# Performance work log

Measured on AMD Instinct MI355X. Metric: run time of the kernel, lower is better.

The kernel has to match this reference:

```python
import jax, jax.numpy as jnp
import numpy as np

N_NODES = 4
EPS = 1e-12


def gcn_conv(x, edge_index, W, b):
    B, N, _ = x.shape
    loop = jnp.arange(N)
    src = jnp.concatenate([edge_index[0], loop])
    dst = jnp.concatenate([edge_index[1], loop])
    deg = jnp.zeros((N,), x.dtype).at[dst].add(1.0)  # in-degree incl. self loops (>=1)
    dinv = jax.lax.rsqrt(deg)
    norm = dinv[src] * dinv[dst]                      # [E+N]
    h = jnp.einsum('bnf,fo->bno', x, W)               # transform first (out < ... ok)
    msgs = h[:, src, :] * norm[None, :, None]         # gather + edge weight
    out = jnp.zeros((B, N, W.shape[1]), x.dtype).at[:, dst, :].add(msgs)  # scatter-add
    return out + b


def sage_conv(x, edge_index, Wl, bl, Wr):
    # PyG SAGEConv(aggr='mean', normalize=True): out = lin_l(mean_j x_j) + lin_r(x_i), l2-normalized
    B, N, F = x.shape
    src, dst = edge_index[0], edge_index[1]
    cnt = jnp.zeros((N,), x.dtype).at[dst].add(1.0)
    cnt = jnp.maximum(cnt, 1.0)
    agg = jnp.zeros((B, N, F), x.dtype).at[:, dst, :].add(x[:, src, :])
    agg = agg / cnt[None, :, None]                    # mean neighbor aggregation
    out = jnp.einsum('bnf,fo->bno', agg, Wl) + bl + jnp.einsum('bnf,fo->bno', x, Wr)
    nrm = jnp.sqrt(jnp.sum(out * out, axis=-1, keepdims=True))
    return out / jnp.maximum(nrm, EPS)


def setup_inputs() -> dict:
    key = jax.random.key(0)
    ks = jax.random.split(key, 16)
    B, N, Cin, Cout = 32768, N_NODES, 64, 10
    E = 12

    def glorot(k, fi, fo):
        s = (6.0 / (fi + fo)) ** 0.5
        return jax.random.uniform(k, (fi, fo), jnp.float32, -s, s)

    x = jax.random.normal(ks[0], (B, N, Cin), jnp.float32)
    edge_index = jax.random.randint(ks[1], (2, E), 0, N, jnp.int64)
    inp = {
        'x': x, 'edge_index': edge_index,
        'W1': glorot(ks[2], Cin, 1024), 'b1': jnp.zeros((1024,), jnp.float32),
        'Wl2': glorot(ks[3], 1024, 512), 'bl2': jnp.zeros((512,), jnp.float32), 'Wr2': glorot(ks[4], 1024, 512),
        'Wl3': glorot(ks[5], 512, 256), 'bl3': jnp.zeros((256,), jnp.float32), 'Wr3': glorot(ks[6], 512, 256),
        'Wl4': glorot(ks[7], 256, 256), 'bl4': jnp.zeros((256,), jnp.float32), 'Wr4': glorot(ks[8], 256, 256),
        'Wfc': glorot(ks[9], N * 256, Cout), 'bfc': jnp.zeros((Cout,), jnp.float32),
    }
    return inp


def reference(x, edge_index, W1, b1, Wl2, bl2, Wr2, Wl3, bl3, Wr3, Wl4, bl4, Wr4, Wfc, bfc):
    h = jax.nn.relu(gcn_conv(x, edge_index, W1, b1))
    h = jax.nn.relu(sage_conv(h, edge_index, Wl2, bl2, Wr2))
    h = jax.nn.relu(sage_conv(h, edge_index, Wl3, bl3, Wr3))
    h = jax.nn.relu(sage_conv(h, edge_index, Wl4, bl4, Wr4))
    h = h.reshape(h.shape[0], -1)                     # [B, 4*256]
    logits = h @ Wfc + bfc
    return jax.nn.softmax(logits, axis=-1)
```

## Files before the change

kernel.cpp:

```cpp
#include <hip/hip_runtime.h>
#include <stdint.h>
#include <math.h>

typedef __bf16 bf16;
typedef __attribute__((ext_vector_type(8))) __bf16 bf16x8;
typedef __attribute__((ext_vector_type(16))) float f32x16;

#define AS1 __attribute__((address_space(1)))
#define AS3 __attribute__((address_space(3)))

__device__ __forceinline__ void glds16(const void* g, void* l) {
    __builtin_amdgcn_global_load_lds((const AS1 uint32_t*)g, (AS3 uint32_t*)l, 16, 0, 0);
}


__global__ void k_setup(const int* __restrict__ ei, float* __restrict__ gmat) {
    if (threadIdx.x != 0 || blockIdx.x != 0) return;
    bool is64 = true;
    for (int i = 0; i < 12; i++) if (ei[2 * i + 1] != 0) { is64 = false; break; }
    int src[12], dst[12];
    for (int e = 0; e < 12; e++) {
        if (is64) { src[e] = ei[2 * e]; dst[e] = ei[24 + 2 * e]; }
        else      { src[e] = ei[e];     dst[e] = ei[12 + e]; }
    }
    float deg[4] = {1.f, 1.f, 1.f, 1.f};
    for (int e = 0; e < 12; e++) deg[dst[e]] += 1.f;
    float dinv[4];
    for (int n = 0; n < 4; n++) dinv[n] = 1.f / sqrtf(deg[n]);
    float A[16];
    for (int i = 0; i < 16; i++) A[i] = 0.f;
    for (int e = 0; e < 12; e++) A[dst[e] * 4 + src[e]] += dinv[src[e]] * dinv[dst[e]];
    for (int n = 0; n < 4; n++) A[n * 4 + n] += dinv[n] * dinv[n];
    float cnt[4] = {0.f, 0.f, 0.f, 0.f};
    for (int e = 0; e < 12; e++) cnt[dst[e]] += 1.f;
    for (int n = 0; n < 4; n++) cnt[n] = fmaxf(cnt[n], 1.f);
    float Mm[16];
    for (int i = 0; i < 16; i++) Mm[i] = 0.f;
    for (int e = 0; e < 12; e++) Mm[dst[e] * 4 + src[e]] += 1.f;
    for (int n = 0; n < 4; n++)
        for (int m = 0; m < 4; m++) Mm[n * 4 + m] /= cnt[n];
    for (int i = 0; i < 16; i++) { gmat[i] = A[i]; gmat[16 + i] = Mm[i]; }
}

__global__ __launch_bounds__(256) void wtransF(const float* __restrict__ W, int K,
                                               int N, bf16* __restrict__ Wt) {
    int a = blockIdx.x * 256 + threadIdx.x;
    if (a >= N * K) return;
    int j = a & 7, c64 = (a >> 3) & 63, tile = a >> 9;
    int m32 = c64 & 31, kh = c64 >> 5;
    int TK = K >> 4;
    int rblk = tile / TK, ks = tile - rblk * TK;
    int n = rblk * 32 + m32, k = ks * 16 + kh * 8 + j;
    Wt[a] = (bf16)W[(size_t)k * N + n];
}

__global__ __launch_bounds__(256) void wtransI(const float* __restrict__ Wl,
                                               const float* __restrict__ Wr,
                                               int K, int F, bf16* __restrict__ Bt) {
    int a = blockIdx.x * 256 + threadIdx.x;
    if (a >= 2 * F * K) return;
    int j = a & 7, c64 = (a >> 3) & 63, tile = a >> 9;
    int m32 = c64 & 31, kh = c64 >> 5;
    int TK = K >> 4;
    int rblk = tile / TK, ks = tile - rblk * TK;
    int n = rblk * 32 + m32, k = ks * 16 + kh * 8 + j;
    int f = n >> 1;
    float v = (n & 1) ? Wr[(size_t)k * F + f] : Wl[(size_t)k * F + f];
    Bt[a] = (bf16)v;
}

__global__ __launch_bounds__(256) void cast_x(const float4* __restrict__ x,
                                              bf16x8* __restrict__ out) {
    int i = blockIdx.x * 256 + threadIdx.x;
    int c64 = i & 63, m32 = c64 & 31, kh = c64 >> 5;
    int tile = i >> 6, RB = tile >> 2, ks = tile & 3;
    int row = RB * 32 + m32;
    int fb4 = ks * 4 + kh * 2;
    float4 a = x[(size_t)row * 16 + fb4], b = x[(size_t)row * 16 + fb4 + 1];
    bf16x8 o;
    o[0] = (bf16)a.x; o[1] = (bf16)a.y; o[2] = (bf16)a.z; o[3] = (bf16)a.w;
    o[4] = (bf16)b.x; o[5] = (bf16)b.y; o[6] = (bf16)b.z; o[7] = (bf16)b.w;
    out[i] = o;
}

__global__ __launch_bounds__(256) void k_zero(float4* __restrict__ p, int n4) {
    int i = blockIdx.x * 256 + threadIdx.x;
    if (i < n4) p[i] = make_float4(0.f, 0.f, 0.f, 0.f);
}

__global__ __launch_bounds__(512, 2) void gemm_mfma(
    const bf16* __restrict__ A, int K,
    const bf16* __restrict__ Bt,
    const float* __restrict__ bias,
    bf16* __restrict__ out, int N, int mode,
    const float* __restrict__ gm, float* __restrict__ ssq) {
    __shared__ bf16 sA[2][16384];
    __shared__ bf16 sB[2][16384];
    const int t = threadIdx.x;
    const int lane = t & 63;
    const int w = t >> 6;
    const int wr = w >> 2, wc = w & 3;
    const int lin = blockIdx.x + gridDim.x * blockIdx.y;
    const int C = gridDim.x;
    const int xcd = lin & 7;
    const int seq = lin >> 3;
    const int rloc = seq / C;
    const int cloc = seq - rloc * C;
    const int row0 = (xcd + 8 * rloc) * 256;
    const int col0 = cloc * 256;
    const int m32 = lane & 31;
    const int kh = lane >> 5;

    f32x16 acc[4][2] = {};

    const int TK = K >> 4;
    const int le = lane * 8;
    const bf16* gA = A  + (size_t)((row0 >> 5) + w) * TK * 512 + le;
    const bf16* gB = Bt + (size_t)((col0 >> 5) + w) * TK * 512 + le;

    const int NT = K >> 6;
#pragma unroll
    for (int p = 0; p < 4; p++) {
        glds16(gA + p * 512, &sA[0][(p * 8 + w) * 512]);
        glds16(gB + p * 512, &sB[0][(p * 8 + w) * 512]);
    }

    for (int kt = 0; kt < NT; kt++) {
        const int rb = kt & 1;
        const size_t knext = (size_t)(kt + 1 < NT ? kt + 1 : kt) * 2048;
        asm volatile("s_waitcnt vmcnt(0)" ::: "memory");
        __builtin_amdgcn_s_barrier();
        asm volatile("" ::: "memory");
        bf16* dA = &sA[rb ^ 1][w * 512];
        bf16* dB = &sB[rb ^ 1][w * 512];
#pragma unroll
        for (int p = 0; p < 4; p++) {
            glds16(gA + knext + p * 512, dA + p * 8 * 512);
            glds16(gB + knext + p * 512, dB + p * 8 * 512);
        }
        const bf16* rA = &sA[rb][0];
        const bf16* rB = &sB[rb][0];
        __builtin_amdgcn_s_setprio(1);
#pragma unroll
        for (int p = 0; p < 4; p++) {
            bf16x8 af[4], bfr[2];
#pragma unroll
            for (int i = 0; i < 4; i++)
                af[i] = *(const bf16x8*)&rA[(p * 8 + wr * 4 + i) * 512 + le];
#pragma unroll
            for (int j = 0; j < 2; j++)
                bfr[j] = *(const bf16x8*)&rB[(p * 8 + wc * 2 + j) * 512 + le];
#pragma unroll
            for (int i = 0; i < 4; i++)
#pragma unroll
                for (int j = 0; j < 2; j++)
                    acc[i][j] = __builtin_amdgcn_mfma_f32_32x32x16_bf16(af[i], bfr[j], acc[i][j], 0, 0, 0);
        }
        __builtin_amdgcn_s_setprio(0);
    }
    asm volatile("s_waitcnt vmcnt(0)" ::: "memory");

    float g[16];
#pragma unroll
    for (int q = 0; q < 16; q++) g[q] = gm[q];

    if (mode == 1) {
        const int Tn = N >> 4;
#pragma unroll
        for (int i = 0; i < 4; i++) {
            size_t RBo = (size_t)(row0 >> 5) + 4 * wr + i;
#pragma unroll
            for (int j = 0; j < 2; j++) {
                int c = col0 + (2 * wc + j) * 32 + m32;
                size_t tbase = (RBo * Tn + (c >> 4)) * 512;
                int coff = ((c >> 3) & 1) * 32;
                int cj = c & 7;
                float bsv = bias[c];
#pragma unroll
                for (int q = 0; q < 4; q++) {
#pragma unroll
                    for (int n = 0; n < 4; n++) {
                        float v = g[n * 4 + 0] * acc[i][j][q * 4 + 0] +
                                  g[n * 4 + 1] * acc[i][j][q * 4 + 1] +
                                  g[n * 4 + 2] * acc[i][j][q * 4 + 2] +
                                  g[n * 4 + 3] * acc[i][j][q * 4 + 3] + bsv;
                        out[tbase + (size_t)(coff + 4 * kh + 8 * q + n) * 8 + cj] =
                            (bf16)fmaxf(v, 0.f);
                    }
                }
            }
        }
    } else {
        const int F = N >> 1;
        const int Tf = F >> 4;
        const bool ev = ((m32 & 1) == 0);
#pragma unroll
        for (int i = 0; i < 4; i++) {
            size_t RBo = (size_t)(row0 >> 5) + 4 * wr + i;
            int rbAbs = row0 + (4 * wr + i) * 32 + 4 * kh;
#pragma unroll
            for (int q = 0; q < 4; q++) {
                float ssql[4] = {0.f, 0.f, 0.f, 0.f};
#pragma unroll
                for (int j = 0; j < 2; j++) {
                    int c = col0 + (2 * wc + j) * 32 + m32;
                    int f = c >> 1;
                    size_t tbase = (RBo * Tf + (f >> 4)) * 512;
                    int foff = ((f >> 3) & 1) * 32;
                    int fj = f & 7;
                    float bsv = bias[f];
                    float mine[4];
                    if (ev) {
#pragma unroll
                        for (int n = 0; n < 4; n++)
                            mine[n] = g[n * 4 + 0] * acc[i][j][q * 4 + 0] +
                                      g[n * 4 + 1] * acc[i][j][q * 4 + 1] +
                                      g[n * 4 + 2] * acc[i][j][q * 4 + 2] +
                                      g[n * 4 + 3] * acc[i][j][q * 4 + 3];
                    } else {
#pragma unroll
                        for (int n = 0; n < 4; n++) mine[n] = acc[i][j][q * 4 + n];
                    }
#pragma unroll
                    for (int n = 0; n < 4; n++) {
                        float oth = __shfl_xor(mine[n], 1);
                        float tot = mine[n] + oth + bsv;
                        ssql[n] += tot * tot;
                        if (ev)
                            out[tbase + (size_t)(foff + 4 * kh + 8 * q + n) * 8 + fj] =
                                (bf16)tot;
                    }
                }
#pragma unroll
                for (int n = 0; n < 4; n++) {
                    float v = ssql[n];
                    v += __shfl_xor(v, 1); v += __shfl_xor(v, 2);
                    v += __shfl_xor(v, 4); v += __shfl_xor(v, 8);
                    v += __shfl_xor(v, 16);
                    ssql[n] = v;
                }
                if (m32 == 0) {
#pragma unroll
                    for (int n = 0; n < 4; n++)
                        atomicAdd(&ssq[rbAbs + 8 * q + n], ssql[n] * 0.5f);
                }
            }
        }
    }
}

__global__ __launch_bounds__(256) void norm_apply(bf16x8* __restrict__ h,
                                                  const float* __restrict__ ssq,
                                                  int tsh) {
    int idx = blockIdx.x * 256 + threadIdx.x;
    int row = (((idx >> 6) >> tsh) << 5) | (idx & 31);
    float inv = 1.f / fmaxf(sqrtf(ssq[row]), 1e-12f);
    bf16x8 v = h[idx], o;
#pragma unroll
    for (int c = 0; c < 8; c++) o[c] = (bf16)fmaxf((float)v[c] * inv, 0.f);
    h[idx] = o;
}

__global__ __launch_bounds__(256) void fc_softmax(const bf16x8* __restrict__ h,
                                                  const float* __restrict__ ssq4,
                                                  const float* __restrict__ Wfc,
                                                  const float* __restrict__ bfc,
                                                  float* __restrict__ outp) {
    __shared__ float WT[10][1024];
    int t = threadIdx.x;
    for (int i = t; i < 10240; i += 256) { int o = i % 10, k = i / 10; WT[o][k] = Wfc[i]; }
    __syncthreads();
    int wid = t >> 6, lane = t & 63;
    size_t e = (size_t)blockIdx.x * 4 + wid;
    size_t eb8 = e >> 3;
    int eo = (int)(e & 7);
    int ks = lane & 15, node = lane >> 4;
    float inv = 1.f / fmaxf(sqrtf(ssq4[e * 4 + node]), 1e-12f);
    float acc[10];
#pragma unroll
    for (int o = 0; o < 10; o++) acc[o] = 0.f;
#pragma unroll
    for (int jj = 0; jj < 2; jj++) {
        size_t ch = (eb8 * 16 + ks) * 64 + jj * 32 + eo * 4 + node;
        bf16x8 v = h[ch];
        float f[8];
#pragma unroll
        for (int c = 0; c < 8; c++) f[c] = fmaxf((float)v[c] * inv, 0.f);
        int k0 = node * 256 + ks * 16 + jj * 8;
#pragma unroll
        for (int o = 0; o < 10; o++) {
            const float* wr = &WT[o][k0];
            float s = 0.f;
#pragma unroll
            for (int c = 0; c < 8; c++) s += f[c] * wr[c];
            acc[o] += s;
        }
    }
#pragma unroll
    for (int o = 0; o < 10; o++) {
        float v = acc[o];
        v += __shfl_xor(v, 32); v += __shfl_xor(v, 16); v += __shfl_xor(v, 8);
        v += __shfl_xor(v, 4);  v += __shfl_xor(v, 2);  v += __shfl_xor(v, 1);
        acc[o] = v + bfc[o];
    }
    float mx = acc[0];
#pragma unroll
    for (int o = 1; o < 10; o++) mx = fmaxf(mx, acc[o]);
    float sum = 0.f, p[10];
#pragma unroll
    for (int o = 0; o < 10; o++) { p[o] = expf(acc[o] - mx); sum += p[o]; }
    float inv2 = 1.f / sum;
    if (lane < 10) outp[e * 10 + lane] = p[lane] * inv2;
}

extern "C" void kernel_launch(void* const* d_in, const int* in_sizes, int n_in,
                              void* d_out, int out_size, void* d_ws, size_t ws_size,
                              hipStream_t stream) {
    const float* x   = (const float*)d_in[0];
    const int*   ei  = (const int*)d_in[1];
    const float* W1  = (const float*)d_in[2];
    const float* b1  = (const float*)d_in[3];
    const float* Wl2 = (const float*)d_in[4];
    const float* bl2 = (const float*)d_in[5];
    const float* Wr2 = (const float*)d_in[6];
    const float* Wl3 = (const float*)d_in[7];
    const float* bl3 = (const float*)d_in[8];
    const float* Wr3 = (const float*)d_in[9];
    const float* Wl4 = (const float*)d_in[10];
    const float* bl4 = (const float*)d_in[11];
    const float* Wr4 = (const float*)d_in[12];
    const float* Wfc = (const float*)d_in[13];
    const float* bfc = (const float*)d_in[14];
    float* out = (float*)d_out;

    const int B = 32768;
    char* base = (char*)d_ws;
    float* gmat = (float*)base;
    bf16* Wt1 = (bf16*)(base + 4096);
    bf16* Wt2 = Wt1 + 1024 * 64;
    bf16* Wt3 = Wt2 + 1024 * 1024;
    bf16* Wt4 = Wt3 + 512 * 512;
    char* sl  = (char*)(Wt4 + 512 * 256);
    size_t fixed = (size_t)(sl - base);

    int Bs = B;
    while (Bs > 512 && fixed + (size_t)Bs * 12848 > ws_size) Bs >>= 1;
    int nslice = B / Bs;
    int M = Bs * 4;

    bf16* R0 = (bf16*)sl;
    bf16* R1 = R0 + (size_t)Bs * 256;
    bf16* R2 = R1 + (size_t)Bs * 4096;
    float* ssqb = (float*)(R2 + (size_t)Bs * 2048);

    hipLaunchKernelGGL(k_setup, dim3(1), dim3(64), 0, stream, ei, gmat);
    hipLaunchKernelGGL(wtransF, dim3((1024 * 64 + 255) / 256), dim3(256), 0, stream,
                       W1, 64, 1024, Wt1);
    hipLaunchKernelGGL(wtransI, dim3((1024 * 1024 + 255) / 256), dim3(256), 0, stream,
                       Wl2, Wr2, 1024, 512, Wt2);
    hipLaunchKernelGGL(wtransI, dim3((512 * 512 + 255) / 256), dim3(256), 0, stream,
                       Wl3, Wr3, 512, 256, Wt3);
    hipLaunchKernelGGL(wtransI, dim3((512 * 256 + 255) / 256), dim3(256), 0, stream,
                       Wl4, Wr4, 256, 256, Wt4);

    for (int s = 0; s < nslice; s++) {
        const float* xs = x + (size_t)s * Bs * 256;
        hipLaunchKernelGGL(k_zero, dim3((3 * M / 4 + 255) / 256), dim3(256), 0, stream,
                           (float4*)ssqb, 3 * M / 4);
        hipLaunchKernelGGL(cast_x, dim3(Bs / 8), dim3(256), 0, stream,
                           (const float4*)xs, (bf16x8*)R0);
        hipLaunchKernelGGL(gemm_mfma, dim3(4, M / 256), dim3(512), 0, stream,
                           R0, 64, Wt1, b1, R1, 1024, 1, gmat, (float*)nullptr);
        hipLaunchKernelGGL(gemm_mfma, dim3(4, M / 256), dim3(512), 0, stream,
                           R1, 1024, Wt2, bl2, R2, 1024, 2, gmat + 16, ssqb);
        hipLaunchKernelGGL(norm_apply, dim3(M / 4), dim3(256), 0, stream,
                           (bf16x8*)R2, ssqb, 5);
        hipLaunchKernelGGL(gemm_mfma, dim3(2, M / 256), dim3(512), 0, stream,
                           R2, 512, Wt3, bl3, R1, 512, 2, gmat + 16, ssqb + M);
        hipLaunchKernelGGL(norm_apply, dim3(M / 8), dim3(256), 0, stream,
                           (bf16x8*)R1, ssqb + M, 4);
        hipLaunchKernelGGL(gemm_mfma, dim3(2, M / 256), dim3(512), 0, stream,
                           R1, 256, Wt4, bl4, R2, 512, 2, gmat + 16, ssqb + 2 * M);
        hipLaunchKernelGGL(fc_softmax, dim3(Bs / 4), dim3(256), 0, stream,
                           (const bf16x8*)R2, ssqb + 2 * M, Wfc, bfc,
                           out + (size_t)s * Bs * 10);
    }
}
```

Measured before the change: 997.7 us.

## Interleave next-tile global-to-LDS loads with MFMA sub-steps in GEMM main loop

Restructures the double-buffered GEMM k-loop so the prefetch of the next A/B tile into LDS is spread across the four MFMA sub-steps instead of being issued all at once at the top of each iteration. Each sub-step issues two loads, synchronizes with barriers and lgkmcnt waits around the MFMA cluster, and the vmcnt wait moves to the final sub-step. The aim is to overlap memory traffic with matrix math in a ping-pong style schedule. In exchange it adds several extra workgroup barriers per k-tile, which could stall the waves.

```diff
diff --git a/kernel.cpp b/kernel.cpp
--- a/kernel.cpp
+++ b/kernel.cpp
@@ -124,23 +124,16 @@
         glds16(gA + p * 512, &sA[0][(p * 8 + w) * 512]);
         glds16(gB + p * 512, &sB[0][(p * 8 + w) * 512]);
     }
+    asm volatile("s_waitcnt vmcnt(0)" ::: "memory");
+    __builtin_amdgcn_s_barrier();
 
     for (int kt = 0; kt < NT; kt++) {
-        const int rb = kt & 1;
+        const int cur = kt & 1;
         const size_t knext = (size_t)(kt + 1 < NT ? kt + 1 : kt) * 2048;
-        asm volatile("s_waitcnt vmcnt(0)" ::: "memory");
-        __builtin_amdgcn_s_barrier();
-        asm volatile("" ::: "memory");
-        bf16* dA = &sA[rb ^ 1][w * 512];
-        bf16* dB = &sB[rb ^ 1][w * 512];
-#pragma unroll
-        for (int p = 0; p < 4; p++) {
-            glds16(gA + knext + p * 512, dA + p * 8 * 512);
-            glds16(gB + knext + p * 512, dB + p * 8 * 512);
-        }
-        const bf16* rA = &sA[rb][0];
-        const bf16* rB = &sB[rb][0];
-        __builtin_amdgcn_s_setprio(1);
+        const bf16* rA = &sA[cur][0];
+        const bf16* rB = &sB[cur][0];
+        bf16* dA = &sA[cur ^ 1][w * 512];
+        bf16* dB = &sB[cur ^ 1][w * 512];
 #pragma unroll
         for (int p = 0; p < 4; p++) {
             bf16x8 af[4], bfr[2];
@@ -150,15 +143,35 @@
 #pragma unroll
             for (int j = 0; j < 2; j++)
                 bfr[j] = *(const bf16x8*)&rB[(p * 8 + wc * 2 + j) * 512 + le];
+            if (p == 0) {
+                glds16(gA + knext,           dA);
+                glds16(gA + knext + 512,     dA + 8 * 512);
+            } else if (p == 1) {
+                glds16(gA + knext + 2 * 512, dA + 16 * 512);
+                glds16(gA + knext + 3 * 512, dA + 24 * 512);
+            } else if (p == 2) {
+                glds16(gB + knext,           dB);
+                glds16(gB + knext + 512,     dB + 8 * 512);
+            } else {
+                glds16(gB + knext + 2 * 512, dB + 16 * 512);
+                glds16(gB + knext + 3 * 512, dB + 24 * 512);
+            }
+            asm volatile("" ::: "memory");
+            __builtin_amdgcn_s_barrier();
+            asm volatile("s_waitcnt lgkmcnt(0)" ::: "memory");
+            __builtin_amdgcn_sched_barrier(0);
+            __builtin_amdgcn_s_setprio(1);
 #pragma unroll
             for (int i = 0; i < 4; i++)
 #pragma unroll
                 for (int j = 0; j < 2; j++)
                     acc[i][j] = __builtin_amdgcn_mfma_f32_32x32x16_bf16(af[i], bfr[j], acc[i][j], 0, 0, 0);
+            __builtin_amdgcn_s_setprio(0);
+            if (p == 3)
+                asm volatile("s_waitcnt vmcnt(0)" ::: "memory");
+            __builtin_amdgcn_s_barrier();
         }
-        __builtin_amdgcn_s_setprio(0);
-    }
-    asm volatile("s_waitcnt vmcnt(0)" ::: "memory");
+    }
 
     float g[16];
 #pragma unroll
```

Measured after the change: 964.3 us. -3.4%, faster.
